# Performance work log

Hardware: AMD Instinct MI355X
Metric: run time of the kernel (lower is better)

## Reference

```python
import jax, jax.numpy as jnp
import numpy as np

V, D, H, L, S = 32000, 1024, 16, 8, 2048
B, T = 2, 1024
HD = D // H


def setup_inputs() -> dict:
    key = jax.random.key(0)
    ks = iter(jax.random.split(key, 16))
    w = lambda shape: jax.random.normal(next(ks), shape, jnp.float32) * 0.02
    return {
        "input_ids": jax.random.randint(next(ks), (B, T), 0, V),
        "text_emb": w((V, D)),
        "pos_emb": w((S, D)),
        "qkv_w": w((L, 3 * D, D)), "qkv_b": jnp.zeros((L, 3 * D)),
        "out_w": w((L, D, D)), "out_b": jnp.zeros((L, D)),
        "ln1_w": jnp.ones((L, D)), "ln1_b": jnp.zeros((L, D)),
        "ln2_w": jnp.ones((L, D)), "ln2_b": jnp.zeros((L, D)),
        "w1": w((L, 4 * D, D)), "b1": jnp.zeros((L, 4 * D)),
        "w2": w((L, D, 4 * D)), "b2": jnp.zeros((L, D)),
        "lnf_w": jnp.ones((D,)), "lnf_b": jnp.zeros((D,)),
        "lm_head_w": w((V, D)),
    }


def layer_norm(x, g, b, eps=1e-5):
    m = jnp.mean(x, -1, keepdims=True)
    v = jnp.var(x, -1, keepdims=True)  # biased var, matches torch LayerNorm
    return (x - m) * jax.lax.rsqrt(v + eps) * g + b


def decoder_block(x, p):
    qkv_w, qkv_b, out_w, out_b, ln1_w, ln1_b, ln2_w, ln2_b, w1, b1, w2, b2 = p
    b_, t_, _ = x.shape
    h = layer_norm(x, ln1_w, ln1_b)
    qkv = h @ qkv_w.T + qkv_b                       # [B,T,3D]
    q, k, v = jnp.split(qkv, 3, axis=-1)
    split = lambda a: a.reshape(b_, t_, H, HD).transpose(0, 2, 1, 3)  # [B,H,T,hd]
    q, k, v = split(q), split(k), split(v)
    scores = jnp.einsum('bhqd,bhkd->bhqk', q, k) * (HD ** -0.5)
    mask = jnp.tril(jnp.ones((t_, t_), bool))
    scores = jnp.where(mask, scores, -jnp.inf)
    attn = jax.nn.softmax(scores, axis=-1)
    o = jnp.einsum('bhqk,bhkd->bhqd', attn, v)
    o = o.transpose(0, 2, 1, 3).reshape(b_, t_, D)
    x = x + o @ out_w.T + out_b
    h = layer_norm(x, ln2_w, ln2_b)
    ff = jax.nn.gelu(h @ w1.T + b1, approximate=False) @ w2.T + b2
    return x + ff


def reference(input_ids, text_emb, pos_emb, qkv_w, qkv_b, out_w, out_b,
              ln1_w, ln1_b, ln2_w, ln2_b, w1, b1, w2, b2,
              lnf_w, lnf_b, lm_head_w):
    t_ = input_ids.shape[1]
    x = text_emb[input_ids] + pos_emb[:t_]          # [B,T,D]
    layer_params = (qkv_w, qkv_b, out_w, out_b, ln1_w, ln1_b,
                    ln2_w, ln2_b, w1, b1, w2, b2)
    def step(x, p):
        return decoder_block(x, p), None
    x, _ = jax.lax.scan(step, x, layer_params)
    x = layer_norm(x, lnf_w, lnf_b)
    logits = x @ lm_head_w.T                        # [B,T,V]
    return logits
```

## Files before the change

### kernel.cpp

```cpp
#include <hip/hip_runtime.h>
#include <hip/hip_bf16.h>

#define Hn 16
#define Dm 1024
#define HDm 64
#define Tn 1024
#define NT 2048
#define Ln 8
#define Vn 32000
#define DFF 4096

typedef unsigned short u16;
typedef unsigned short ushort8 __attribute__((ext_vector_type(8)));
typedef __bf16 bf16x8 __attribute__((ext_vector_type(8)));
typedef float f32x4 __attribute__((ext_vector_type(4)));

__device__ __forceinline__ float b2f(u16 u) {
    union { unsigned int i; float f; } x; x.i = ((unsigned int)u) << 16; return x.f;
}
__device__ __forceinline__ u16 f2b(float f) {
    union { float f; unsigned int i; } x; x.f = f;
    unsigned int r = x.i + 0x7FFFu + ((x.i >> 16) & 1u);
    return (u16)(r >> 16);
}
__device__ __forceinline__ float inload(const void* p, size_t idx, bool isBf) {
    return isBf ? b2f(((const u16*)p)[idx]) : ((const float*)p)[idx];
}

__device__ __forceinline__ void gload16(const void* g, void* l) {
    const unsigned int __attribute__((address_space(1)))* gp =
        (const unsigned int __attribute__((address_space(1)))*)(unsigned long long)g;
    unsigned int __attribute__((address_space(3)))* lp =
        (unsigned int __attribute__((address_space(3)))*)(unsigned int)(unsigned long long)l;
    __builtin_amdgcn_global_load_lds(gp, lp, 16, 0, 0);
}

__global__ __launch_bounds__(256) void sniff_k(const void* temb, int* flag)
{
    int tid = threadIdx.x;
    const u16* p = (const u16*)temb;
    int cnt = 0;
    for (int i = tid; i < 4096; i += 256) {
        float v = b2f(p[2 * i]);
        if (!(fabsf(v) < 8.0f)) cnt++;
    }
    __shared__ int red[256];
    red[tid] = cnt;
    __syncthreads();
    for (int st = 128; st > 0; st >>= 1) {
        if (tid < st) red[tid] += red[tid + st];
        __syncthreads();
    }
    if (tid == 0) flag[0] = (red[0] < 8) ? 1 : 0;
}

__global__ __launch_bounds__(256) void conv_k(
    const void* __restrict__ src, u16* __restrict__ dst, const int* __restrict__ flagp)
{
    if (flagp[0] != 0) return;
    size_t i = ((size_t)blockIdx.x * 256 + threadIdx.x) * 8;
    const float* s = (const float*)src + i;
    f32x4 a = *(const f32x4*)s;
    f32x4 b = *(const f32x4*)(s + 4);
    ushort8 o;
    o[0]=f2b(a[0]); o[1]=f2b(a[1]); o[2]=f2b(a[2]); o[3]=f2b(a[3]);
    o[4]=f2b(b[0]); o[5]=f2b(b[1]); o[6]=f2b(b[2]); o[7]=f2b(b[3]);
    *(ushort8*)(dst + i) = o;
}

__global__ __launch_bounds__(256) void embed_k(
    const int* __restrict__ ids, const void* __restrict__ temb,
    const void* __restrict__ pemb, float* __restrict__ x,
    const int* __restrict__ flagp)
{
    const bool isBf = flagp[0] != 0;
    int n = blockIdx.x;
    int t = n & (Tn - 1);
    int id = ids[n];
    int d = threadIdx.x * 4;
    float* xo = x + (size_t)n * Dm + d;
#pragma unroll
    for (int j = 0; j < 4; ++j)
        xo[j] = inload(temb, (size_t)id * Dm + d + j, isBf)
              + inload(pemb, (size_t)t  * Dm + d + j, isBf);
}

__global__ __launch_bounds__(256) void ln_k(
    const float* __restrict__ x, const void* __restrict__ g,
    const void* __restrict__ bta, size_t goff, u16* __restrict__ hout,
    const int* __restrict__ flagp)
{
    const bool isBf = flagp[0] != 0;
    int n = blockIdx.x;
    int tid = threadIdx.x;
    const float* xr = x + (size_t)n * Dm;
    f32x4 v = *(const f32x4*)&xr[tid * 4];
    float s = v[0] + v[1] + v[2] + v[3];
    float ss = v[0]*v[0] + v[1]*v[1] + v[2]*v[2] + v[3]*v[3];
    __shared__ float r1[256], r2[256];
    r1[tid] = s; r2[tid] = ss;
    __syncthreads();
    for (int st = 128; st > 0; st >>= 1) {
        if (tid < st) { r1[tid] += r1[tid + st]; r2[tid] += r2[tid + st]; }
        __syncthreads();
    }
    float mean = r1[0] * (1.0f / Dm);
    float var  = r2[0] * (1.0f / Dm) - mean * mean;
    float rs = rsqrtf(var + 1e-5f);
    u16* ho = hout + (size_t)n * Dm + tid * 4;
#pragma unroll
    for (int j = 0; j < 4; ++j) {
        float gv = inload(g,   goff + tid * 4 + j, isBf);
        float bv = inload(bta, goff + tid * 4 + j, isBf);
        ho[j] = f2b((v[j] - mean) * rs * gv + bv);
    }
}

__global__ __launch_bounds__(256) void lnfuse_k(
    float* __restrict__ x, const float* __restrict__ P, int nP,
    const void* __restrict__ g, const void* __restrict__ bta, size_t goff,
    u16* __restrict__ hout, const int* __restrict__ flagp)
{
    const bool isBf = flagp[0] != 0;
    int n = blockIdx.x;
    int tid = threadIdx.x;
    float* xr = x + (size_t)n * Dm;
    f32x4 v = *(const f32x4*)&xr[tid * 4];
    if (nP == 2) {
        const float* p0 = P + (size_t)n * Dm;
        const float* p1 = P + (size_t)NT * Dm + (size_t)n * Dm;
        f32x4 a = *(const f32x4*)&p0[tid * 4];
        f32x4 b = *(const f32x4*)&p1[tid * 4];
#pragma unroll
        for (int j = 0; j < 4; ++j) v[j] = v[j] + a[j] + b[j];
        *(f32x4*)&xr[tid * 4] = v;
    }
    float s = v[0] + v[1] + v[2] + v[3];
    float ss = v[0]*v[0] + v[1]*v[1] + v[2]*v[2] + v[3]*v[3];
    __shared__ float r1[256], r2[256];
    r1[tid] = s; r2[tid] = ss;
    __syncthreads();
    for (int st = 128; st > 0; st >>= 1) {
        if (tid < st) { r1[tid] += r1[tid + st]; r2[tid] += r2[tid + st]; }
        __syncthreads();
    }
    float mean = r1[0] * (1.0f / Dm);
    float var  = r2[0] * (1.0f / Dm) - mean * mean;
    float rs = rsqrtf(var + 1e-5f);
    u16* ho = hout + (size_t)n * Dm + tid * 4;
#pragma unroll
    for (int j = 0; j < 4; ++j) {
        float gv = inload(g,   goff + tid * 4 + j, isBf);
        float bv = inload(bta, goff + tid * 4 + j, isBf);
        ho[j] = f2b((v[j] - mean) * rs * gv + bv);
    }
}

template<int EPI>
__global__ __launch_bounds__(256) void gemm_k(
    const u16* __restrict__ A, const void* __restrict__ Bw, size_t woff,
    const void* __restrict__ bias, size_t boff,
    u16* __restrict__ Obf, float* __restrict__ Xres, void* __restrict__ Oext,
    const int* __restrict__ flagp, int M, int N, int K)
{
    const bool isBf = flagp[0] != 0;
    __shared__ __align__(16) u16 As[128][40];
    __shared__ __align__(16) u16 Bs[128][40];
    const int tid  = threadIdx.x;
    const int lane = tid & 63;
    const int wave = tid >> 6;
    const int wr = (wave >> 1) * 64;
    const int wc = (wave & 1) * 64;
    const int row0 = blockIdx.y * 128;
    const int col0 = blockIdx.x * 128;
    const int lr = lane & 15;
    const int lk = (lane >> 4) * 8;
    const int sr = tid >> 2;
    const int sc = (tid & 3) * 8;

    f32x4 acc[4][4] = {};

    for (int k0 = 0; k0 < K; k0 += 32) {
#pragma unroll
        for (int i = 0; i < 2; ++i) {
            int r = sr + i * 64;
            *(ushort8*)&As[r][sc] = *(const ushort8*)&A[(size_t)(row0 + r) * K + k0 + sc];
            size_t be = woff + (size_t)(col0 + r) * K + k0 + sc;
            if (isBf) {
                *(ushort8*)&Bs[r][sc] = *(const ushort8*)&((const u16*)Bw)[be];
            } else {
                const float* src = (const float*)Bw + be;
                f32x4 v0 = *(const f32x4*)src;
                f32x4 v1 = *(const f32x4*)(src + 4);
                ushort8 tv;
                tv[0]=f2b(v0[0]); tv[1]=f2b(v0[1]); tv[2]=f2b(v0[2]); tv[3]=f2b(v0[3]);
                tv[4]=f2b(v1[0]); tv[5]=f2b(v1[1]); tv[6]=f2b(v1[2]); tv[7]=f2b(v1[3]);
                *(ushort8*)&Bs[r][sc] = tv;
            }
        }
        __syncthreads();
        bf16x8 af[4], bfr[4];
#pragma unroll
        for (int m = 0; m < 4; ++m) af[m]  = *(const bf16x8*)&As[wr + m * 16 + lr][lk];
#pragma unroll
        for (int n = 0; n < 4; ++n) bfr[n] = *(const bf16x8*)&Bs[wc + n * 16 + lr][lk];
#pragma unroll
        for (int m = 0; m < 4; ++m)
#pragma unroll
            for (int n = 0; n < 4; ++n)
                acc[m][n] = __builtin_amdgcn_mfma_f32_16x16x32_bf16(af[m], bfr[n], acc[m][n], 0, 0, 0);
        __syncthreads();
    }

    const int rbase = row0 + wr + (lane >> 4) * 4;
    const int cbase = col0 + wc + lr;
#pragma unroll
    for (int n = 0; n < 4; ++n) {
        int c = cbase + n * 16;
        float bv = (bias != nullptr) ? inload(bias, boff + c, isBf) : 0.0f;
#pragma unroll
        for (int m = 0; m < 4; ++m) {
#pragma unroll
            for (int j = 0; j < 4; ++j) {
                int r = rbase + m * 16 + j;
                float v = acc[m][n][j] + bv;
                if (EPI == 1) v = 0.5f * v * (1.0f + erff(v * 0.70710678118f));
                size_t idx = (size_t)r * N + c;
                if (EPI == 2) {
                    Xres[idx] = Xres[idx] + v;
                } else if (EPI == 3) {
                    if (isBf) ((u16*)Oext)[idx] = f2b(v);
                    else      ((float*)Oext)[idx] = v;
                } else {
                    Obf[idx] = f2b(v);
                }
            }
        }
    }
}

template<int EPI>
__global__ __launch_bounds__(256) void gemm2p_k(
    const u16* __restrict__ A, const void* __restrict__ Worig, size_t woff,
    const u16* __restrict__ Wws,
    const void* __restrict__ bias, size_t boff,
    u16* __restrict__ Obf, float* __restrict__ Xres, void* __restrict__ Oext,
    const int* __restrict__ flagp, int N, int Kstride, int Kloop, int nChunk)
{
    const bool isBf = flagp[0] != 0;
    const u16* __restrict__ W = isBf ? ((const u16*)Worig + woff) : Wws;

    __shared__ __align__(16) u16 As[2][128][32];
    __shared__ __align__(16) u16 Bs[2][128][32];

    const int totalT = (N >> 7) * 16;
    const int full = totalT * nChunk;
    const int bid = blockIdx.x;
    const int sidall = (bid & 7) * (full >> 3) + (bid >> 3);
    const int chunk = sidall / totalT;
    const int sid = sidall - chunk * totalT;
    const int row0 = (sid & 15) * 128;
    const int col0 = (sid >> 4) * 128;
    const int kbase = chunk * Kloop;

    const int tid  = threadIdx.x;
    const int lane = tid & 63;
    const int wv   = tid >> 6;
    const int wr = (wv >> 1) * 64;
    const int wc = (wv & 1) * 64;
    const int lr = lane & 15;
    const int lk = (lane >> 4) * 8;
    const int srow = lane >> 2;
    const int scol = (lane & 3) * 8;

    f32x4 acc[4][4] = {};

    auto STAGE = [&](int bb, int k0) {
#pragma unroll
        for (int i = 0; i < 2; ++i) {
            const int r = i * 64 + wv * 16;
            gload16(&A[(size_t)(row0 + r + srow) * Kstride + kbase + k0 + scol], &As[bb][r][0]);
            gload16(&W[(size_t)(col0 + r + srow) * Kstride + kbase + k0 + scol], &Bs[bb][r][0]);
        }
    };

    STAGE(0, 0);
    __syncthreads();
    int cur = 0;
    for (int k0 = 0; k0 < Kloop; k0 += 32) {
        if (k0 + 32 < Kloop) STAGE(cur ^ 1, k0 + 32);
        bf16x8 af[4], bfr[4];
#pragma unroll
        for (int m = 0; m < 4; ++m) af[m]  = *(const bf16x8*)&As[cur][wr + m * 16 + lr][lk];
#pragma unroll
        for (int n = 0; n < 4; ++n) bfr[n] = *(const bf16x8*)&Bs[cur][wc + n * 16 + lr][lk];
#pragma unroll
        for (int m = 0; m < 4; ++m)
#pragma unroll
            for (int n = 0; n < 4; ++n)
                acc[m][n] = __builtin_amdgcn_mfma_f32_16x16x32_bf16(af[m], bfr[n], acc[m][n], 0, 0, 0);
        __syncthreads();
        cur ^= 1;
    }

    const int rbase = row0 + wr + (lane >> 4) * 4;
    const int cbase = col0 + wc + lr;
#pragma unroll
    for (int n = 0; n < 4; ++n) {
        int c = cbase + n * 16;
        float bv = (bias != nullptr && chunk == 0) ? inload(bias, boff + c, isBf) : 0.0f;
#pragma unroll
        for (int m = 0; m < 4; ++m) {
#pragma unroll
            for (int j = 0; j < 4; ++j) {
                int r = rbase + m * 16 + j;
                float v = acc[m][n][j] + bv;
                if (EPI == 1) v = 0.5f * v * (1.0f + erff(v * 0.70710678118f));
                size_t idx = (size_t)r * N + c;
                if (EPI == 2) {
                    Xres[idx] = Xres[idx] + v;
                } else if (EPI == 4) {
                    ((float*)Oext)[(size_t)chunk * NT * N + idx] = v;
                } else {
                    Obf[idx] = f2b(v);
                }
            }
        }
    }
}

template<int EPI>
__global__ __launch_bounds__(512, 2) void gemm3_k(
    const u16* __restrict__ A, const void* __restrict__ Worig, size_t woff,
    const u16* __restrict__ Wws,
    const void* __restrict__ bias, size_t boff,
    u16* __restrict__ Obf, float* __restrict__ Xres, void* __restrict__ Oext,
    const int* __restrict__ flagp, int N, int K)
{
    const bool isBf = flagp[0] != 0;
    const u16* __restrict__ W = isBf ? ((const u16*)Worig + woff) : Wws;

    __shared__ __align__(16) u16 As[2][256][64];
    __shared__ __align__(16) u16 Bs[2][256][64];

    const int total = (N >> 8) * 8;
    const int bid = blockIdx.x;
    const int sid = (bid & 7) * (total >> 3) + (bid >> 3);
    const int row0 = (sid & 7) * 256;
    const int col0 = (sid >> 3) * 256;

    const int tid  = threadIdx.x;
    const int lane = tid & 63;
    const int wv   = tid >> 6;
    const int wm   = wv >> 2;
    const int wn   = wv & 3;
    const int lr   = lane & 15;
    const int lk   = (lane >> 4) * 8;
    const int grow = lane >> 3;
    const int gcol = (lane & 7) * 8;

    f32x4 acc[8][4] = {};

    auto STAGE = [&](int bb, int k0) {
#pragma unroll
        for (int j = 0; j < 4; ++j) {
            const int r = j * 64 + wv * 8;
            gload16(&A[(size_t)(row0 + r + grow) * K + k0 + gcol], &As[bb][r][0]);
            gload16(&W[(size_t)(col0 + r + grow) * K + k0 + gcol], &Bs[bb][r][0]);
        }
    };

    STAGE(0, 0);
    __syncthreads();
    int cur = 0;
    for (int k0 = 0; k0 < K; k0 += 64) {
        if (k0 + 64 < K) STAGE(cur ^ 1, k0 + 64);
#pragma unroll
        for (int kk = 0; kk < 2; ++kk) {
            bf16x8 af[8], bfr[4];
#pragma unroll
            for (int m = 0; m < 8; ++m)
                af[m] = *(const bf16x8*)&As[cur][wm * 128 + m * 16 + lr][kk * 32 + lk];
#pragma unroll
            for (int n = 0; n < 4; ++n)
                bfr[n] = *(const bf16x8*)&Bs[cur][wn * 64 + n * 16 + lr][kk * 32 + lk];
#pragma unroll
            for (int m = 0; m < 8; ++m)
#pragma unroll
                for (int n = 0; n < 4; ++n)
                    acc[m][n] = __builtin_amdgcn_mfma_f32_16x16x32_bf16(af[m], bfr[n], acc[m][n], 0, 0, 0);
        }
        __syncthreads();
        cur ^= 1;
    }

    const int rbase = row0 + wm * 128 + (lane >> 4) * 4;
    const int cbase = col0 + wn * 64 + lr;
#pragma unroll
    for (int n = 0; n < 4; ++n) {
        int c = cbase + n * 16;
        float bv = (bias != nullptr) ? inload(bias, boff + c, isBf) : 0.0f;
#pragma unroll
        for (int m = 0; m < 8; ++m) {
#pragma unroll
            for (int j = 0; j < 4; ++j) {
                int r = rbase + m * 16 + j;
                float v = acc[m][n][j] + bv;
                size_t idx = (size_t)r * N + c;
                if (EPI == 3) {
                    if (isBf) ((u16*)Oext)[idx] = f2b(v);
                    else      ((float*)Oext)[idx] = v;
                } else {
                    Obf[idx] = f2b(v);
                }
            }
        }
    }
}

__global__ __launch_bounds__(256) void fattn_k(
    const u16* __restrict__ qkv, u16* __restrict__ attn)
{
    __shared__ __align__(16) u16 Ks[32][72];
    __shared__ __align__(16) u16 Vt[64][40];
    __shared__ __align__(16) u16 Ps[4][16][40];

    const int bid  = blockIdx.x;
    const int pair = bid & 7;
    const int h    = (bid >> 3) & 15;
    const int b    = bid >> 7;
    const int tid  = threadIdx.x;
    const int lane = tid & 63;
    const int wv   = tid >> 6;
    const int lr   = lane & 15;
    const int g    = lane >> 4;
    const int lk   = g * 8;

    const size_t base = (size_t)b * Tn * 3 * Dm + (size_t)h * HDm;
    const int srow = tid >> 3;
    const int sc8  = (tid & 7) * 8;

    for (int half = 0; half < 2; ++half) {
        const int jt = (half == 0) ? pair : 15 - pair;
        const int q0 = jt * 64 + wv * 16;

        bf16x8 aq[2];
#pragma unroll
        for (int kh = 0; kh < 2; ++kh)
            aq[kh] = *(const bf16x8*)&qkv[base + (size_t)(q0 + lr) * (3 * Dm) + kh * 32 + lk];

        f32x4 o[4] = {};
        float mrun[4], lrun[4];
#pragma unroll
        for (int j = 0; j < 4; ++j) { mrun[j] = -3e38f; lrun[j] = 0.0f; }

        const int nkv = 2 * jt + 2;
        for (int it = 0; it < nkv; ++it) {
            const int kv0 = it * 32;
            __syncthreads();
            {
                const size_t rbase = base + (size_t)(kv0 + srow) * (3 * Dm);
                *(ushort8*)&Ks[srow][sc8] = *(const ushort8*)&qkv[rbase + Dm + sc8];
                ushort8 vvv = *(const ushort8*)&qkv[rbase + 2 * Dm + sc8];
#pragma unroll
                for (int jj = 0; jj < 8; ++jj) Vt[sc8 + jj][srow] = vvv[jj];
            }
            __syncthreads();

            f32x4 s[2] = {};
#pragma unroll
            for (int kh = 0; kh < 2; ++kh) {
#pragma unroll
                for (int n = 0; n < 2; ++n) {
                    bf16x8 bk = *(const bf16x8*)&Ks[n * 16 + lr][kh * 32 + lk];
                    s[n] = __builtin_amdgcn_mfma_f32_16x16x32_bf16(aq[kh], bk, s[n], 0, 0, 0);
                }
            }

            float scale[4];
#pragma unroll
            for (int j = 0; j < 4; ++j) {
                const int qrow = q0 + g * 4 + j;
                float v0 = (kv0 + lr      <= qrow) ? s[0][j] * 0.125f : -3e38f;
                float v1 = (kv0 + 16 + lr <= qrow) ? s[1][j] * 0.125f : -3e38f;
                float rm = fmaxf(v0, v1);
#pragma unroll
                for (int msk = 1; msk < 16; msk <<= 1)
                    rm = fmaxf(rm, __shfl_xor(rm, msk));
                float mnew = fmaxf(mrun[j], rm);
                scale[j] = __expf(mrun[j] - mnew);
                float p0 = __expf(v0 - mnew);
                float p1 = __expf(v1 - mnew);
                s[0][j] = p0; s[1][j] = p1;
                float rs = p0 + p1;
#pragma unroll
                for (int msk = 1; msk < 16; msk <<= 1)
                    rs += __shfl_xor(rs, msk);
                lrun[j] = lrun[j] * scale[j] + rs;
                mrun[j] = mnew;
            }

#pragma unroll
            for (int n = 0; n < 2; ++n)
#pragma unroll
                for (int j = 0; j < 4; ++j)
                    Ps[wv][g * 4 + j][n * 16 + lr] = f2b(s[n][j]);
            bf16x8 ap = *(const bf16x8*)&Ps[wv][lr][lk];

#pragma unroll
            for (int d = 0; d < 4; ++d) {
                f32x4 c = o[d];
#pragma unroll
                for (int j = 0; j < 4; ++j) c[j] *= scale[j];
                bf16x8 bv = *(const bf16x8*)&Vt[d * 16 + lr][lk];
                o[d] = __builtin_amdgcn_mfma_f32_16x16x32_bf16(ap, bv, c, 0, 0, 0);
            }
        }

#pragma unroll
        for (int d = 0; d < 4; ++d) {
#pragma unroll
            for (int j = 0; j < 4; ++j) {
                const int qrow = q0 + g * 4 + j;
                attn[(size_t)(b * Tn + qrow) * Dm + h * HDm + d * 16 + lr] =
                    f2b(o[d][j] / lrun[j]);
            }
        }
    }
}

extern "C" void kernel_launch(void* const* d_in, const int* in_sizes, int n_in,
                              void* d_out, int out_size, void* d_ws, size_t ws_size,
                              hipStream_t stream)
{
    const int*  ids       = (const int*)d_in[0];
    const void* text_emb  = d_in[1];
    const void* pos_emb   = d_in[2];
    const void* qkv_w     = d_in[3];
    const void* qkv_b     = d_in[4];
    const void* out_w     = d_in[5];
    const void* out_b     = d_in[6];
    const void* ln1_w     = d_in[7];
    const void* ln1_b     = d_in[8];
    const void* ln2_w     = d_in[9];
    const void* ln2_b     = d_in[10];
    const void* w1        = d_in[11];
    const void* b1        = d_in[12];
    const void* w2        = d_in[13];
    const void* b2        = d_in[14];
    const void* lnf_w     = d_in[15];
    const void* lnf_b     = d_in[16];
    const void* lm_head_w = d_in[17];

    char* ws = (char*)d_ws;
    size_t used = 0;
    auto carve = [&](size_t bytes) { char* p = ws + used; used += (bytes + 15) & ~15ull; return p; };

    int*   flag = (int*)  carve(16);
    float* x    = (float*)carve((size_t)NT * Dm * 4);
    u16*   h    = (u16*)  carve((size_t)NT * Dm * 2);
    u16*   qkv  = (u16*)  carve((size_t)NT * 3 * Dm * 2);
    u16*   attn = (u16*)  carve((size_t)NT * Dm * 2);
    u16*   u    = (u16*)  carve((size_t)NT * DFF * 2);

    float* Pf = (float*)qkv;
    float* Pa = (float*)u;

    const size_t nLM  = (size_t)Vn * Dm;
    const size_t nQKV = (size_t)Ln * 3 * Dm * Dm;
    const size_t nOUT = (size_t)Ln * Dm * Dm;
    const size_t nW1  = (size_t)Ln * DFF * Dm;
    const size_t nW2  = (size_t)Ln * Dm * DFF;

    u16* wsLM  = (u16*)carve(nLM * 2);
    size_t lm_used = used;
    u16* wsQKV = (u16*)carve(nQKV * 2);
    u16* wsOUT = (u16*)carve(nOUT * 2);
    u16* wsW1  = (u16*)carve(nW1 * 2);
    u16* wsW2  = (u16*)carve(nW2 * 2);
    size_t all_used = used;

    const int tier = (ws_size >= all_used) ? 2 : (ws_size >= lm_used ? 1 : 0);

    dim3 blk(256);

    sniff_k<<<1, blk, 0, stream>>>(text_emb, flag);

    if (tier >= 1)
        conv_k<<<nLM / 2048, blk, 0, stream>>>(lm_head_w, wsLM, flag);
    if (tier == 2) {
        conv_k<<<nQKV / 2048, blk, 0, stream>>>(qkv_w, wsQKV, flag);
        conv_k<<<nOUT / 2048, blk, 0, stream>>>(out_w, wsOUT, flag);
        conv_k<<<nW1  / 2048, blk, 0, stream>>>(w1,    wsW1,  flag);
        conv_k<<<nW2  / 2048, blk, 0, stream>>>(w2,    wsW2,  flag);
    }

    embed_k<<<NT, blk, 0, stream>>>(ids, text_emb, pos_emb, x, flag);

    if (tier == 2) {
        for (int l = 0; l < Ln; ++l) {
            size_t oQW = (size_t)l * 3 * Dm * Dm, oQB = (size_t)l * 3 * Dm;
            size_t oOW = (size_t)l * Dm * Dm,     oOB = (size_t)l * Dm;
            size_t oW1 = (size_t)l * DFF * Dm,    oB1 = (size_t)l * DFF;
            size_t oW2 = (size_t)l * Dm * DFF,    oB2 = (size_t)l * Dm;
            size_t oLN = (size_t)l * Dm;

            lnfuse_k<<<NT, blk, 0, stream>>>(x, Pf, (l == 0) ? 0 : 2,
                                             ln1_w, ln1_b, oLN, h, flag);
            gemm2p_k<0><<<16 * (3 * Dm / 128), blk, 0, stream>>>(
                h, qkv_w, oQW, wsQKV + oQW, qkv_b, oQB, qkv, nullptr, nullptr,
                flag, 3 * Dm, Dm, Dm, 1);
            fattn_k<<<2 * Hn * 8, blk, 0, stream>>>(qkv, attn);
            gemm2p_k<4><<<2 * 16 * (Dm / 128), blk, 0, stream>>>(
                attn, out_w, oOW, wsOUT + oOW, out_b, oOB, nullptr, nullptr, Pa,
                flag, Dm, Dm, Dm / 2, 2);
            lnfuse_k<<<NT, blk, 0, stream>>>(x, Pa, 2, ln2_w, ln2_b, oLN, h, flag);
            gemm2p_k<1><<<16 * (DFF / 128), blk, 0, stream>>>(
                h, w1, oW1, wsW1 + oW1, b1, oB1, u, nullptr, nullptr,
                flag, DFF, Dm, Dm, 1);
            gemm2p_k<4><<<2 * 16 * (Dm / 128), blk, 0, stream>>>(
                u, w2, oW2, wsW2 + oW2, b2, oB2, nullptr, nullptr, Pf,
                flag, Dm, DFF, DFF / 2, 2);
        }
        lnfuse_k<<<NT, blk, 0, stream>>>(x, Pf, 2, lnf_w, lnf_b, 0, h, flag);
        gemm3_k<3><<<8 * (Vn / 256), dim3(512), 0, stream>>>(
            h, lm_head_w, 0, wsLM, nullptr, 0, nullptr, nullptr, d_out, flag, Vn, Dm);
    } else {
        for (int l = 0; l < Ln; ++l) {
            size_t oQW = (size_t)l * 3 * Dm * Dm, oQB = (size_t)l * 3 * Dm;
            size_t oOW = (size_t)l * Dm * Dm,     oOB = (size_t)l * Dm;
            size_t oW1 = (size_t)l * DFF * Dm,    oB1 = (size_t)l * DFF;
            size_t oW2 = (size_t)l * Dm * DFF,    oB2 = (size_t)l * Dm;
            size_t oLN = (size_t)l * Dm;

            ln_k<<<NT, blk, 0, stream>>>(x, ln1_w, ln1_b, oLN, h, flag);
            gemm_k<0><<<dim3(3 * Dm / 128, NT / 128), blk, 0, stream>>>(
                h, qkv_w, oQW, qkv_b, oQB, qkv, nullptr, nullptr, flag, NT, 3 * Dm, Dm);
            fattn_k<<<2 * Hn * 8, blk, 0, stream>>>(qkv, attn);
            gemm_k<2><<<dim3(Dm / 128, NT / 128), blk, 0, stream>>>(
                attn, out_w, oOW, out_b, oOB, nullptr, x, nullptr, flag, NT, Dm, Dm);
            ln_k<<<NT, blk, 0, stream>>>(x, ln2_w, ln2_b, oLN, h, flag);
            gemm_k<1><<<dim3(DFF / 128, NT / 128), blk, 0, stream>>>(
                h, w1, oW1, b1, oB1, u, nullptr, nullptr, flag, NT, DFF, Dm);
            gemm_k<2><<<dim3(Dm / 128, NT / 128), blk, 0, stream>>>(
                u, w2, oW2, b2, oB2, nullptr, x, nullptr, flag, NT, Dm, DFF);
        }
        ln_k<<<NT, blk, 0, stream>>>(x, lnf_w, lnf_b, 0, h, flag);
        if (tier == 1)
            gemm3_k<3><<<8 * (Vn / 256), dim3(512), 0, stream>>>(
                h, lm_head_w, 0, wsLM, nullptr, 0, nullptr, nullptr, d_out, flag, Vn, Dm);
        else
            gemm_k<3><<<dim3(Vn / 128, NT / 128), blk, 0, stream>>>(
                h, lm_head_w, 0, nullptr, 0, nullptr, nullptr, d_out, flag, NT, Vn, Dm);
    }
}
```

Measured before the change: 2.204 ms.

## Replace attention kernel with pre-transposed V and per-wave 16-row flash attention

Adds a kernel that transposes V per head into a scratch buffer, reusing the h buffer, so the attention PV MFMA can read contiguous V columns straight from global memory. A new single-wave flash attention kernel handles 16 query rows per block over 2048 blocks, with heavy causal tiles scheduled first. This gives much finer parallelism than the old 256-block kernel and drops the shared-memory K/V staging. In exchange it adds one extra kernel launch and a V round trip through memory, and K/V loads are no longer shared across waves. The other edits are signature cleanup.

```diff
diff --git a/kernel.cpp b/kernel.cpp
--- a/kernel.cpp
+++ b/kernel.cpp
@@ -244,7 +244,7 @@
     const u16* __restrict__ A, const void* __restrict__ Worig, size_t woff,
     const u16* __restrict__ Wws,
     const void* __restrict__ bias, size_t boff,
-    u16* __restrict__ Obf, float* __restrict__ Xres, void* __restrict__ Oext,
+    u16* __restrict__ Obf, float* __restrict__ Xres, float* __restrict__ OextA,
     const int* __restrict__ flagp, int N, int Kstride, int Kloop, int nChunk)
 {
     const bool isBf = flagp[0] != 0;
@@ -320,7 +320,7 @@
                 if (EPI == 2) {
                     Xres[idx] = Xres[idx] + v;
                 } else if (EPI == 4) {
-                    ((float*)Oext)[(size_t)chunk * NT * N + idx] = v;
+                    OextA[(size_t)chunk * NT * N + idx] = v;
                 } else {
                     Obf[idx] = f2b(v);
                 }
@@ -334,7 +334,7 @@
     const u16* __restrict__ A, const void* __restrict__ Worig, size_t woff,
     const u16* __restrict__ Wws,
     const void* __restrict__ bias, size_t boff,
-    u16* __restrict__ Obf, float* __restrict__ Xres, void* __restrict__ Oext,
+    u16* __restrict__ Obf, void* __restrict__ Oext,
     const int* __restrict__ flagp, int N, int K)
 {
     const bool isBf = flagp[0] != 0;
@@ -416,6 +416,122 @@
             }
         }
     }
+}
+
+__global__ __launch_bounds__(256) void vtrans_k(
+    const u16* __restrict__ qkv, u16* __restrict__ vt)
+{
+    __shared__ __align__(16) u16 til[64][72];
+    const int bid = blockIdx.x;
+    const int kt = bid & 15;
+    const int bh = bid >> 4;
+    const int b = bh >> 4, hh = bh & 15;
+    const int tid = threadIdx.x;
+    const int r = tid >> 2;
+    const int c = (tid & 3) * 16;
+    const u16* src = qkv + (size_t)(b * Tn + kt * 64 + r) * (3 * Dm) + 2 * Dm + hh * HDm + c;
+    *(ushort8*)&til[r][c]     = *(const ushort8*)&src[0];
+    *(ushort8*)&til[r][c + 8] = *(const ushort8*)&src[8];
+    __syncthreads();
+    u16* dst = vt + (size_t)(bh * HDm + r) * Tn + kt * 64 + c;
+    ushort8 o1, o2;
+#pragma unroll
+    for (int j = 0; j < 8; ++j) { o1[j] = til[c + j][r]; o2[j] = til[c + 8 + j][r]; }
+    *(ushort8*)&dst[0] = o1;
+    *(ushort8*)&dst[8] = o2;
+}
+
+__global__ __launch_bounds__(64) void fattn2_k(
+    const u16* __restrict__ qkv, const u16* __restrict__ vt, u16* __restrict__ attn)
+{
+    __shared__ __align__(16) u16 Ps[16][40];
+
+    const int bid = blockIdx.x;
+    const int bh  = bid & 31;
+    const int qt  = 63 - (bid >> 5);
+    const int b = bh >> 4, hh = bh & 15;
+    const int lane = threadIdx.x;
+    const int lr = lane & 15;
+    const int g  = lane >> 4;
+    const int lk = g * 8;
+
+    const size_t qbase = (size_t)b * Tn * 3 * Dm + (size_t)hh * HDm;
+    const int q0 = qt * 16;
+
+    bf16x8 aq[2];
+#pragma unroll
+    for (int kh = 0; kh < 2; ++kh)
+        aq[kh] = *(const bf16x8*)&qkv[qbase + (size_t)(q0 + lr) * (3 * Dm) + kh * 32 + lk];
+
+    f32x4 o[4] = {};
+    float mrun[4], lrun[4];
+#pragma unroll
+    for (int j = 0; j < 4; ++j) { mrun[j] = -3e38f; lrun[j] = 0.0f; }
+
+    const u16* kp  = qkv + qbase + Dm;
+    const u16* vtp = vt + (size_t)(bh * HDm) * Tn;
+
+    const int nkv = (qt >> 1) + 1;
+    for (int it = 0; it < nkv; ++it) {
+        const int kv0 = it * 32;
+
+        f32x4 s[2] = {};
+#pragma unroll
+        for (int n = 0; n < 2; ++n)
+#pragma unroll
+            for (int kh = 0; kh < 2; ++kh) {
+                bf16x8 bk = *(const bf16x8*)&kp[(size_t)(kv0 + n * 16 + lr) * (3 * Dm) + kh * 32 + lk];
+                s[n] = __builtin_amdgcn_mfma_f32_16x16x32_bf16(aq[kh], bk, s[n], 0, 0, 0);
+            }
+
+        float scale[4];
+#pragma unroll
+        for (int j = 0; j < 4; ++j) {
+            const int qrow = q0 + g * 4 + j;
+            float v0 = (kv0 + lr      <= qrow) ? s[0][j] * 0.125f : -3e38f;
+            float v1 = (kv0 + 16 + lr <= qrow) ? s[1][j] * 0.125f : -3e38f;
+            float rm = fmaxf(v0, v1);
+#pragma unroll
+            for (int msk = 1; msk < 16; msk <<= 1)
+                rm = fmaxf(rm, __shfl_xor(rm, msk));
+            float mnew = fmaxf(mrun[j], rm);
+            scale[j] = __expf(mrun[j] - mnew);
+            float p0 = __expf(v0 - mnew);
+            float p1 = __expf(v1 - mnew);
+            s[0][j] = p0; s[1][j] = p1;
+            float rs = p0 + p1;
+#pragma unroll
+            for (int msk = 1; msk < 16; msk <<= 1)
+                rs += __shfl_xor(rs, msk);
+            lrun[j] = lrun[j] * scale[j] + rs;
+            mrun[j] = mnew;
+        }
+
+#pragma unroll
+        for (int n = 0; n < 2; ++n)
+#pragma unroll
+            for (int j = 0; j < 4; ++j)
+                Ps[g * 4 + j][n * 16 + lr] = f2b(s[n][j]);
+        bf16x8 ap = *(const bf16x8*)&Ps[lr][lk];
+
+#pragma unroll
+        for (int d = 0; d < 4; ++d) {
+            f32x4 c = o[d];
+#pragma unroll
+            for (int j = 0; j < 4; ++j) c[j] *= scale[j];
+            bf16x8 bv = *(const bf16x8*)&vtp[(size_t)(d * 16 + lr) * Tn + kv0 + lk];
+            o[d] = __builtin_amdgcn_mfma_f32_16x16x32_bf16(ap, bv, c, 0, 0, 0);
+        }
+    }
+
+#pragma unroll
+    for (int d = 0; d < 4; ++d)
+#pragma unroll
+        for (int j = 0; j < 4; ++j) {
+            const int qrow = q0 + g * 4 + j;
+            attn[(size_t)(b * Tn + qrow) * Dm + hh * HDm + d * 16 + lr] =
+                f2b(o[d][j] / lrun[j]);
+        }
 }
 
 __global__ __launch_bounds__(256) void fattn_k(
@@ -563,6 +679,7 @@
     u16*   attn = (u16*)  carve((size_t)NT * Dm * 2);
     u16*   u    = (u16*)  carve((size_t)NT * DFF * 2);
 
+    u16*   vt = h;
     float* Pf = (float*)qkv;
     float* Pa = (float*)u;
 
@@ -578,9 +695,9 @@
     u16* wsOUT = (u16*)carve(nOUT * 2);
     u16* wsW1  = (u16*)carve(nW1 * 2);
     u16* wsW2  = (u16*)carve(nW2 * 2);
-    size_t all_used = used;
-
-    const int tier = (ws_size >= all_used) ? 2 : (ws_size >= lm_used ? 1 : 0);
+    size_t t2_used = used;
+
+    const int tier = (ws_size >= t2_used) ? 2 : (ws_size >= lm_used ? 1 : 0);
 
     dim3 blk(256);
 
@@ -588,7 +705,7 @@
 
     if (tier >= 1)
         conv_k<<<nLM / 2048, blk, 0, stream>>>(lm_head_w, wsLM, flag);
-    if (tier == 2) {
+    if (tier >= 2) {
         conv_k<<<nQKV / 2048, blk, 0, stream>>>(qkv_w, wsQKV, flag);
         conv_k<<<nOUT / 2048, blk, 0, stream>>>(out_w, wsOUT, flag);
         conv_k<<<nW1  / 2048, blk, 0, stream>>>(w1,    wsW1,  flag);
@@ -597,7 +714,7 @@
 
     embed_k<<<NT, blk, 0, stream>>>(ids, text_emb, pos_emb, x, flag);
 
-    if (tier == 2) {
+    if (tier >= 2) {
         for (int l = 0; l < Ln; ++l) {
             size_t oQW = (size_t)l * 3 * Dm * Dm, oQB = (size_t)l * 3 * Dm;
             size_t oOW = (size_t)l * Dm * Dm,     oOB = (size_t)l * Dm;
@@ -610,7 +727,8 @@
             gemm2p_k<0><<<16 * (3 * Dm / 128), blk, 0, stream>>>(
                 h, qkv_w, oQW, wsQKV + oQW, qkv_b, oQB, qkv, nullptr, nullptr,
                 flag, 3 * Dm, Dm, Dm, 1);
-            fattn_k<<<2 * Hn * 8, blk, 0, stream>>>(qkv, attn);
+            vtrans_k<<<32 * 16, blk, 0, stream>>>(qkv, vt);
+            fattn2_k<<<2048, dim3(64), 0, stream>>>(qkv, vt, attn);
             gemm2p_k<4><<<2 * 16 * (Dm / 128), blk, 0, stream>>>(
                 attn, out_w, oOW, wsOUT + oOW, out_b, oOB, nullptr, nullptr, Pa,
                 flag, Dm, Dm, Dm / 2, 2);
@@ -624,7 +742,7 @@
         }
         lnfuse_k<<<NT, blk, 0, stream>>>(x, Pf, 2, lnf_w, lnf_b, 0, h, flag);
         gemm3_k<3><<<8 * (Vn / 256), dim3(512), 0, stream>>>(
-            h, lm_head_w, 0, wsLM, nullptr, 0, nullptr, nullptr, d_out, flag, Vn, Dm);
+            h, lm_head_w, 0, wsLM, nullptr, 0, nullptr, d_out, flag, Vn, Dm);
     } else {
         for (int l = 0; l < Ln; ++l) {
             size_t oQW = (size_t)l * 3 * Dm * Dm, oQB = (size_t)l * 3 * Dm;
@@ -648,7 +766,7 @@
         ln_k<<<NT, blk, 0, stream>>>(x, lnf_w, lnf_b, 0, h, flag);
         if (tier == 1)
             gemm3_k<3><<<8 * (Vn / 256), dim3(512), 0, stream>>>(
-                h, lm_head_w, 0, wsLM, nullptr, 0, nullptr, nullptr, d_out, flag, Vn, Dm);
+                h, lm_head_w, 0, wsLM, nullptr, 0, nullptr, d_out, flag, Vn, Dm);
         else
             gemm_k<3><<<dim3(Vn / 128, NT / 128), blk, 0, stream>>>(
                 h, lm_head_w, 0, nullptr, 0, nullptr, nullptr, d_out, flag, NT, Vn, Dm);
```

After: 2.217 ms. About the same (+0.6%).
